# Kernel optimization log

Hardware: AMD Instinct MI355X
Metric: run time of the kernel (lower is better)

The kernel has to match this reference:

```python
import jax, jax.numpy as jnp
import numpy as np

NEG_BIG = -9e15
LEAKY_SLOPE = 0.01  # nn.LeakyReLU default

N, IN_DIM, HIDDEN_DIM, OUT_DIM = 16384, 512, 256, 128


def setup_inputs() -> dict:
    key = jax.random.key(0)
    ks = jax.random.split(key, 6)
    # He-ish init scaled like torch Linear defaults (uniform +-1/sqrt(fan_in))
    def lin_init(k, fan_in, fan_out):
        kw, kb = jax.random.split(k)
        bound = 1.0 / np.sqrt(fan_in)
        W = jax.random.uniform(kw, (fan_in, fan_out), jnp.float32, -bound, bound)
        b = jax.random.uniform(kb, (fan_out,), jnp.float32, -bound, bound)
        return W, b
    W1, b1 = lin_init(ks[0], IN_DIM, HIDDEN_DIM)
    W2, b2 = lin_init(ks[1], HIDDEN_DIM, OUT_DIM)
    x = jax.random.normal(ks[2], (N, IN_DIM), jnp.float32)
    return {
        "x": x,
        "g": 0,  # unused graph arg in the executed forward path
        "W1": W1, "b1": b1,
        "W2": W2, "b2": b2,
        "alpha": jnp.array([0.1], jnp.float32),
        "beta": jnp.array([0.9], jnp.float32),
    }


def _sim_agg(x):
    # adj: [N, N] dense similarity
    adj = jnp.matmul(x, x.T)
    a = jnp.where(adj > 0, adj, jnp.float32(NEG_BIG))
    sim1 = jax.nn.softmax(a, axis=1)
    return jnp.matmul(sim1, x)


def reference(x, g, W1, b1, W2, b2, alpha, beta):
    # dropout is inactive in eval mode (F.dropout with training=False)
    h = jnp.matmul(x, W1) + b1
    h = jnp.where(h >= 0, h, LEAKY_SLOPE * h)  # LeakyReLU
    h = jnp.matmul(h, W2) + b2                 # [N, out_dim]
    out = alpha * _sim_agg(h) + beta * h
    return jax.nn.log_softmax(out, axis=1)
```

## Files before the change

### kernel.cpp

```cpp
#include <hip/hip_runtime.h>
#include <hip/hip_bf16.h>

typedef __bf16 bf16_t;
typedef __bf16 bf16x8 __attribute__((ext_vector_type(8)));
typedef __bf16 bf16x4 __attribute__((ext_vector_type(4)));
typedef __bf16 bf16x2 __attribute__((ext_vector_type(2)));
typedef float f32x4 __attribute__((ext_vector_type(4)));
typedef float f32x2 __attribute__((ext_vector_type(2)));
typedef unsigned short u16;

#define NROWS 16384
#define KDIM  512
#define HID   256
#define ODIM  128
#define KS    8

__device__ __forceinline__ f32x4 mfma16(bf16x8 a, bf16x8 b, f32x4 c) {
  return __builtin_amdgcn_mfma_f32_16x16x32_bf16(a, b, c, 0, 0, 0);
}

__device__ __forceinline__ void dma16(const void* g, void* l) {
  __builtin_amdgcn_global_load_lds(
      (const __attribute__((address_space(1))) unsigned int*)g,
      (__attribute__((address_space(3))) unsigned int*)l, 16, 0, 0);
}

__global__ __launch_bounds__(256) void prep(const float* __restrict__ x,
                                            const float* __restrict__ W1,
                                            const float* __restrict__ W2,
                                            bf16_t* __restrict__ xb,
                                            bf16_t* __restrict__ W1T,
                                            bf16_t* __restrict__ W2T) {
  int t = blockIdx.x * 256 + threadIdx.x;
  int stride = gridDim.x * 256;
  for (int e = t; e < NROWS * KDIM / 4; e += stride) {
    f32x4 v = *(const f32x4*)(x + (size_t)e * 4);
    bf16x4 pk;
    pk[0] = (bf16_t)v[0]; pk[1] = (bf16_t)v[1];
    pk[2] = (bf16_t)v[2]; pk[3] = (bf16_t)v[3];
    *(bf16x4*)(xb + (size_t)e * 4) = pk;
  }
  for (int e = t; e < HID * KDIM; e += stride) {
    int n = e >> 9, k = e & 511;
    W1T[e] = (bf16_t)W1[k * HID + n];
  }
  for (int e = t; e < ODIM * HID; e += stride) {
    int n = e >> 8, k = e & 255;
    W2T[e] = (bf16_t)W2[k * ODIM + n];
  }
}

__global__ __launch_bounds__(256) void gemm1(const bf16_t* __restrict__ xb,
                                             const bf16_t* __restrict__ W1T,
                                             const float* __restrict__ b1,
                                             bf16_t* __restrict__ h1) {
  __shared__ u16 As[128 * 40];
  __shared__ u16 Bs[64 * 40];
  int tid = threadIdx.x;
  int lane = tid & 63, w = tid >> 6;
  int r = lane & 15, q = lane >> 4;
  int wm = w & 1, wn = w >> 1;
  int mbase = blockIdx.x * 128, nbase = blockIdx.y * 64;

  f32x4 acc[4][2];
#pragma unroll
  for (int ms = 0; ms < 4; ms++)
#pragma unroll
    for (int ns = 0; ns < 2; ns++) acc[ms][ns] = (f32x4){0.f, 0.f, 0.f, 0.f};

  for (int kb = 0; kb < KDIM; kb += 32) {
#pragma unroll
    for (int i = 0; i < 2; i++) {
      int g = tid + 256 * i;
      int rr = g >> 2, c = (g & 3) * 8;
      *(bf16x8*)&As[rr * 40 + c] =
          *(const bf16x8*)(xb + (size_t)(mbase + rr) * KDIM + kb + c);
    }
    {
      int rr = tid >> 2, c = (tid & 3) * 8;
      *(bf16x8*)&Bs[rr * 40 + c] =
          *(const bf16x8*)(W1T + (size_t)(nbase + rr) * KDIM + kb + c);
    }
    __syncthreads();
    bf16x8 af[4], bfr[2];
#pragma unroll
    for (int ms = 0; ms < 4; ms++)
      af[ms] = *(bf16x8*)&As[(wm * 64 + ms * 16 + r) * 40 + q * 8];
#pragma unroll
    for (int ns = 0; ns < 2; ns++)
      bfr[ns] = *(bf16x8*)&Bs[(wn * 32 + ns * 16 + r) * 40 + q * 8];
#pragma unroll
    for (int ms = 0; ms < 4; ms++)
#pragma unroll
      for (int ns = 0; ns < 2; ns++)
        acc[ms][ns] = mfma16(af[ms], bfr[ns], acc[ms][ns]);
    __syncthreads();
  }
#pragma unroll
  for (int ns = 0; ns < 2; ns++) {
    int col = nbase + wn * 32 + ns * 16 + r;
    float bias = b1[col];
#pragma unroll
    for (int ms = 0; ms < 4; ms++) {
      int row0 = mbase + wm * 64 + ms * 16 + q * 4;
#pragma unroll
      for (int reg = 0; reg < 4; reg++) {
        float v = acc[ms][ns][reg] + bias;
        v = v >= 0.f ? v : 0.01f * v;
        h1[(size_t)(row0 + reg) * HID + col] = (bf16_t)v;
      }
    }
  }
}

__global__ __launch_bounds__(256) void gemm2(const bf16_t* __restrict__ h1,
                                             const bf16_t* __restrict__ W2T,
                                             const float* __restrict__ b2,
                                             bf16_t* __restrict__ hb,
                                             bf16_t* __restrict__ hT) {
  __shared__ u16 As[128 * 40];
  __shared__ u16 Bs[64 * 40];
  int tid = threadIdx.x;
  int lane = tid & 63, w = tid >> 6;
  int r = lane & 15, q = lane >> 4;
  int wm = w & 1, wn = w >> 1;
  int mbase = blockIdx.x * 128, nbase = blockIdx.y * 64;

  f32x4 acc[4][2];
#pragma unroll
  for (int ms = 0; ms < 4; ms++)
#pragma unroll
    for (int ns = 0; ns < 2; ns++) acc[ms][ns] = (f32x4){0.f, 0.f, 0.f, 0.f};

  for (int kb = 0; kb < HID; kb += 32) {
#pragma unroll
    for (int i = 0; i < 2; i++) {
      int g = tid + 256 * i;
      int rr = g >> 2, c = (g & 3) * 8;
      *(bf16x8*)&As[rr * 40 + c] =
          *(const bf16x8*)(h1 + (size_t)(mbase + rr) * HID + kb + c);
    }
    {
      int rr = tid >> 2, c = (tid & 3) * 8;
      *(bf16x8*)&Bs[rr * 40 + c] =
          *(const bf16x8*)(W2T + (size_t)(nbase + rr) * HID + kb + c);
    }
    __syncthreads();
    bf16x8 af[4], bfr[2];
#pragma unroll
    for (int ms = 0; ms < 4; ms++)
      af[ms] = *(bf16x8*)&As[(wm * 64 + ms * 16 + r) * 40 + q * 8];
#pragma unroll
    for (int ns = 0; ns < 2; ns++)
      bfr[ns] = *(bf16x8*)&Bs[(wn * 32 + ns * 16 + r) * 40 + q * 8];
#pragma unroll
    for (int ms = 0; ms < 4; ms++)
#pragma unroll
      for (int ns = 0; ns < 2; ns++)
        acc[ms][ns] = mfma16(af[ms], bfr[ns], acc[ms][ns]);
    __syncthreads();
  }
#pragma unroll
  for (int ns = 0; ns < 2; ns++) {
    int col = nbase + wn * 32 + ns * 16 + r;
    float bias = b2[col];
#pragma unroll
    for (int ms = 0; ms < 4; ms++) {
      int row0 = mbase + wm * 64 + ms * 16 + q * 4;
      bf16x4 pk;
#pragma unroll
      for (int reg = 0; reg < 4; reg++) {
        float v = acc[ms][ns][reg] + bias;
        hb[(size_t)(row0 + reg) * ODIM + col] = (bf16_t)v;
        pk[reg] = (bf16_t)v;
      }
      *(bf16x4*)(hT + (size_t)col * NROWS + row0) = pk;
    }
  }
}

__global__ __launch_bounds__(256, 4) void flash(const bf16_t* __restrict__ hb,
                                                const bf16_t* __restrict__ hT,
                                                bf16_t* __restrict__ OpA,
                                                bf16_t* __restrict__ OpB,
                                                float* __restrict__ Ml) {
  __shared__ __align__(16) u16 KA[8 * 512];
  __shared__ __align__(16) u16 KT[2][8 * 512];
  __shared__ __align__(16) u16 Pm[4 * 32 * 40];

  int tid = threadIdx.x;
  int lane = tid & 63, w = tid >> 6;
  int r = lane & 15, q = lane >> 4;
  int ksplit = blockIdx.x >> 7;
  int qtile = blockIdx.x & 127;
  int qbase = qtile * 128 + w * 32;
  int kbase = ksplit * (NROWS / KS);
  const int niter = (NROWS / KS) / 32;

  const char* gbase;
  size_t jmul;
  int ginc;
  u16* dbase;
  if (w < 2) {
    gbase = (const char*)(hb + (size_t)(kbase + w * 16 + r) * ODIM + q * 8);
    jmul = 32 * 2;
    ginc = 32 * ODIM * 2;
    dbase = KA + w * 4 * 512;
  } else {
    gbase = (const char*)(hT + (size_t)((w - 2) * 64 + r) * NROWS + kbase + q * 8);
    jmul = (size_t)16 * NROWS * 2;
    ginc = 32 * 2;
    dbase = KT[0] + (w - 2) * 4 * 512;
  }

  bf16x8 qf[2][4];
#pragma unroll
  for (int qt = 0; qt < 2; qt++) {
    int qrow = qbase + qt * 16 + r;
#pragma unroll
    for (int kk = 0; kk < 4; kk++)
      qf[qt][kk] = *(const bf16x8*)(hb + (size_t)qrow * ODIM + kk * 32 + q * 8);
  }

  f32x4 oa[8][2];
#pragma unroll
  for (int m8 = 0; m8 < 8; m8++)
#pragma unroll
    for (int qt = 0; qt < 2; qt++) oa[m8][qt] = (f32x4){0.f, 0.f, 0.f, 0.f};
  float m_run[2] = {0.f, 0.f}, l_run[2] = {0.f, 0.f};

#pragma unroll
  for (int j = 0; j < 4; j++) dma16(gbase + j * jmul, dbase + j * 512);
  gbase += ginc;

  for (int it = 0; it < niter; it++) {
    __syncthreads();

    f32x4 s[2][2];
#pragma unroll
    for (int mt = 0; mt < 2; mt++)
#pragma unroll
      for (int qt = 0; qt < 2; qt++) s[mt][qt] = (f32x4){0.f, 0.f, 0.f, 0.f};
#pragma unroll
    for (int mt = 0; mt < 2; mt++)
#pragma unroll
      for (int kk = 0; kk < 4; kk++) {
        bf16x8 af = *(bf16x8*)&KA[(mt * 4 + kk) * 512 + lane * 8];
        s[mt][0] = mfma16(af, qf[0][kk], s[mt][0]);
        s[mt][1] = mfma16(af, qf[1][kk], s[mt][1]);
      }
    __syncthreads();

    if (it + 1 < niter) {
      u16* d = dbase;
      if (w >= 2) d += ((it + 1) & 1) * 4096;
#pragma unroll
      for (int j = 0; j < 4; j++) dma16(gbase + j * jmul, d + j * 512);
      gbase += ginc;
    }

    float mx[2];
#pragma unroll
    for (int qt = 0; qt < 2; qt++) {
      float m = m_run[qt];
#pragma unroll
      for (int mt = 0; mt < 2; mt++)
#pragma unroll
        for (int reg = 0; reg < 4; reg++) {
          float v = s[mt][qt][reg];
          m = v > 0.f ? fmaxf(m, v) : m;
        }
      m = fmaxf(m, __shfl_xor(m, 16, 64));
      m = fmaxf(m, __shfl_xor(m, 32, 64));
      mx[qt] = m;
    }
    if (__any(mx[0] > m_run[0] || mx[1] > m_run[1])) {
      float sc0 = __expf(m_run[0] - mx[0]);
      float sc1 = __expf(m_run[1] - mx[1]);
      m_run[0] = mx[0]; m_run[1] = mx[1];
      l_run[0] *= sc0; l_run[1] *= sc1;
#pragma unroll
      for (int m8 = 0; m8 < 8; m8++)
#pragma unroll
        for (int reg = 0; reg < 4; reg++) {
          oa[m8][0][reg] *= sc0;
          oa[m8][1][reg] *= sc1;
        }
    }
#pragma unroll
    for (int qt = 0; qt < 2; qt++) {
      float rs = 0.f;
      bf16x4 pk[2];
#pragma unroll
      for (int mt = 0; mt < 2; mt++)
#pragma unroll
        for (int reg = 0; reg < 4; reg++) {
          float v = s[mt][qt][reg];
          float p = v > 0.f ? __expf(v - m_run[qt]) : 0.f;
          rs += p;
          pk[mt][reg] = (bf16_t)p;
        }
      rs += __shfl_xor(rs, 16, 64);
      rs += __shfl_xor(rs, 32, 64);
      l_run[qt] += rs;
#pragma unroll
      for (int mt = 0; mt < 2; mt++)
        *(bf16x4*)&Pm[w * 1280 + (qt * 16 + r) * 40 + mt * 16 + q * 4] = pk[mt];
    }

    bf16x8 pf0 = *(bf16x8*)&Pm[w * 1280 + r * 40 + q * 8];
    bf16x8 pf1 = *(bf16x8*)&Pm[w * 1280 + (16 + r) * 40 + q * 8];
    const u16* kt = KT[it & 1];
#pragma unroll
    for (int m8 = 0; m8 < 8; m8++) {
      bf16x8 af = *(bf16x8*)&kt[m8 * 512 + lane * 8];
      oa[m8][0] = mfma16(af, pf0, oa[m8][0]);
      oa[m8][1] = mfma16(af, pf1, oa[m8][1]);
    }
  }

  bf16_t* op = ksplit < 6 ? OpA + (size_t)ksplit * NROWS * ODIM
                          : OpB + (size_t)(ksplit - 6) * NROWS * ODIM;
#pragma unroll
  for (int qt = 0; qt < 2; qt++) {
    int row = qbase + qt * 16 + r;
#pragma unroll
    for (int m8 = 0; m8 < 8; m8++) {
      bf16x4 pk;
#pragma unroll
      for (int reg = 0; reg < 4; reg++) pk[reg] = (bf16_t)oa[m8][qt][reg];
      *(bf16x4*)(op + (size_t)row * ODIM + m8 * 16 + q * 4) = pk;
    }
    if (q == 0) {
      Ml[(ksplit * NROWS + row) * 2 + 0] = m_run[qt];
      Ml[(ksplit * NROWS + row) * 2 + 1] = l_run[qt];
    }
  }
}

__global__ __launch_bounds__(256) void merge_ls(const bf16_t* __restrict__ OpA,
                                                const bf16_t* __restrict__ OpB,
                                                const float* __restrict__ Ml,
                                                const bf16_t* __restrict__ hbf,
                                                const float* __restrict__ alpha_p,
                                                const float* __restrict__ beta_p,
                                                float* __restrict__ out) {
  int tid = threadIdx.x, lane = tid & 63, w = tid >> 6;
  float al = alpha_p[0], be = beta_p[0];
  for (int i = 0; i < 8; i++) {
    int row = blockIdx.x * 32 + w * 8 + i;
    float mk[KS], lk[KS], ak[KS];
    float M = 0.f;
#pragma unroll
    for (int ksp = 0; ksp < KS; ksp++) {
      mk[ksp] = Ml[(ksp * NROWS + row) * 2 + 0];
      lk[ksp] = Ml[(ksp * NROWS + row) * 2 + 1];
      M = fmaxf(M, mk[ksp]);
    }
    float lt = 0.f;
#pragma unroll
    for (int ksp = 0; ksp < KS; ksp++) {
      ak[ksp] = __expf(mk[ksp] - M);
      lt += lk[ksp] * ak[ksp];
    }
    float inv = al / lt;
    int d0 = lane * 2;
    float a0 = 0.f, a1 = 0.f;
#pragma unroll
    for (int ksp = 0; ksp < KS; ksp++) {
      const bf16_t* op = ksp < 6 ? OpA + (size_t)ksp * NROWS * ODIM
                                 : OpB + (size_t)(ksp - 6) * NROWS * ODIM;
      bf16x2 v = *(const bf16x2*)(op + (size_t)row * ODIM + d0);
      a0 += ak[ksp] * (float)v[0];
      a1 += ak[ksp] * (float)v[1];
    }
    bf16x2 hv = *(const bf16x2*)(hbf + (size_t)row * ODIM + d0);
    float v0 = inv * a0 + be * (float)hv[0];
    float v1 = inv * a1 + be * (float)hv[1];
    float mxv = fmaxf(v0, v1);
#pragma unroll
    for (int off = 1; off < 64; off <<= 1) mxv = fmaxf(mxv, __shfl_xor(mxv, off, 64));
    float se = __expf(v0 - mxv) + __expf(v1 - mxv);
#pragma unroll
    for (int off = 1; off < 64; off <<= 1) se += __shfl_xor(se, off, 64);
    float lz = mxv + __logf(se);
    f32x2 st = {v0 - lz, v1 - lz};
    *(f32x2*)(out + (size_t)row * ODIM + d0) = st;
  }
}

extern "C" void kernel_launch(void* const* d_in, const int* in_sizes, int n_in,
                              void* d_out, int out_size, void* d_ws,
                              size_t ws_size, hipStream_t stream) {
  const float* x     = (const float*)d_in[0];
  const float* W1    = (const float*)d_in[2];
  const float* b1    = (const float*)d_in[3];
  const float* W2    = (const float*)d_in[4];
  const float* b2    = (const float*)d_in[5];
  const float* alpha = (const float*)d_in[6];
  const float* beta  = (const float*)d_in[7];

  char* ws = (char*)d_ws;
  bf16_t* xb  = (bf16_t*)(ws + 0);
  bf16_t* W1T = (bf16_t*)(ws + 16777216);
  bf16_t* W2T = (bf16_t*)(ws + 17039360);
  bf16_t* h1  = (bf16_t*)(ws + 17104896);
  bf16_t* hbf = (bf16_t*)(ws + 25493504);
  bf16_t* hT  = (bf16_t*)(ws + 29687808);
  float*  Ml  = (float*)(ws + 33882112);
  bf16_t* OpB = (bf16_t*)(ws + 34930688);
  bf16_t* OpA = (bf16_t*)(ws + 0);
  float* outp = (float*)d_out;

  prep<<<1024, 256, 0, stream>>>(x, W1, W2, xb, W1T, W2T);
  gemm1<<<dim3(128, 4), 256, 0, stream>>>(xb, W1T, b1, h1);
  gemm2<<<dim3(128, 2), 256, 0, stream>>>(h1, W2T, b2, hbf, hT);
  flash<<<128 * KS, 256, 0, stream>>>(hbf, hT, OpA, OpB, Ml);
  merge_ls<<<512, 256, 0, stream>>>(OpA, OpB, Ml, hbf, alpha, beta, outp);
}
```

Measured before the change: 364.3 us.

## Replace online softmax max with Cauchy-Schwarz row bound and double-buffer key tiles

A new rowstat kernel computes each row's squared norm and a global maximum squared norm. The flash kernel then uses the fixed per-row bound sqrt(|h_i|^2 * max|h_j|^2) in place of a running max. This removes the per-iteration max reduction, the cross-lane shuffles and the accumulator rescaling, and it also simplifies the merge step to plain sums. The key tile KA is now double-buffered, which drops one barrier per iteration, and the loop is unrolled by two. The P scratch tile uses an XOR swizzle instead of padding. The risk is exp underflow when the bound sits far above a row's true maximum, plus the cost of an extra small kernel launch and an atomic.

```diff
diff --git a/kernel.cpp b/kernel.cpp
--- a/kernel.cpp
+++ b/kernel.cpp
@@ -30,9 +30,11 @@
                                             const float* __restrict__ W2,
                                             bf16_t* __restrict__ xb,
                                             bf16_t* __restrict__ W1T,
-                                            bf16_t* __restrict__ W2T) {
+                                            bf16_t* __restrict__ W2T,
+                                            float* __restrict__ gmax) {
   int t = blockIdx.x * 256 + threadIdx.x;
   int stride = gridDim.x * 256;
+  if (t == 0) *gmax = 0.f;
   for (int e = t; e < NROWS * KDIM / 4; e += stride) {
     f32x4 v = *(const f32x4*)(x + (size_t)e * 4);
     bf16x4 pk;
@@ -179,14 +181,39 @@
   }
 }
 
+__global__ __launch_bounds__(256) void rowstat(const bf16_t* __restrict__ hb,
+                                               float* __restrict__ Mrow,
+                                               float* __restrict__ gmax) {
+  int row = blockIdx.x * 256 + threadIdx.x;
+  const bf16x8* p = (const bf16x8*)(hb + (size_t)row * ODIM);
+  float n2 = 0.f;
+#pragma unroll
+  for (int i = 0; i < 16; i++) {
+    bf16x8 v = p[i];
+#pragma unroll
+    for (int j = 0; j < 8; j++) {
+      float f = (float)v[j];
+      n2 += f * f;
+    }
+  }
+  Mrow[row] = n2;
+  float m = n2;
+#pragma unroll
+  for (int off = 1; off < 64; off <<= 1) m = fmaxf(m, __shfl_xor(m, off, 64));
+  if ((threadIdx.x & 63) == 0)
+    atomicMax((unsigned int*)gmax, __float_as_uint(m));
+}
+
 __global__ __launch_bounds__(256, 4) void flash(const bf16_t* __restrict__ hb,
                                                 const bf16_t* __restrict__ hT,
+                                                const float* __restrict__ Mrow,
+                                                const float* __restrict__ gmax,
                                                 bf16_t* __restrict__ OpA,
                                                 bf16_t* __restrict__ OpB,
                                                 float* __restrict__ Ml) {
-  __shared__ __align__(16) u16 KA[8 * 512];
-  __shared__ __align__(16) u16 KT[2][8 * 512];
-  __shared__ __align__(16) u16 Pm[4 * 32 * 40];
+  __shared__ __align__(16) u16 KA[2][4096];
+  __shared__ __align__(16) u16 KT[2][4096];
+  __shared__ __align__(16) u16 Pm[4096];
 
   int tid = threadIdx.x;
   int lane = tid & 63, w = tid >> 6;
@@ -195,28 +222,32 @@
   int qtile = blockIdx.x & 127;
   int qbase = qtile * 128 + w * 32;
   int kbase = ksplit * (NROWS / KS);
-  const int niter = (NROWS / KS) / 32;
 
   const char* gbase;
   size_t jmul;
-  int ginc;
-  u16* dbase;
+  long ginc;
+  u16 *d0, *d1;
   if (w < 2) {
     gbase = (const char*)(hb + (size_t)(kbase + w * 16 + r) * ODIM + q * 8);
-    jmul = 32 * 2;
+    jmul = 64;
     ginc = 32 * ODIM * 2;
-    dbase = KA + w * 4 * 512;
+    d0 = &KA[0][w * 2048];
+    d1 = &KA[1][w * 2048];
   } else {
     gbase = (const char*)(hT + (size_t)((w - 2) * 64 + r) * NROWS + kbase + q * 8);
     jmul = (size_t)16 * NROWS * 2;
-    ginc = 32 * 2;
-    dbase = KT[0] + (w - 2) * 4 * 512;
+    ginc = 64;
+    d0 = &KT[0][(w - 2) * 2048];
+    d1 = &KT[1][(w - 2) * 2048];
   }
 
   bf16x8 qf[2][4];
+  float mi[2];
+  float gm = gmax[0];
 #pragma unroll
   for (int qt = 0; qt < 2; qt++) {
     int qrow = qbase + qt * 16 + r;
+    mi[qt] = sqrtf(Mrow[qrow] * gm);
 #pragma unroll
     for (int kk = 0; kk < 4; kk++)
       qf[qt][kk] = *(const bf16x8*)(hb + (size_t)qrow * ODIM + kk * 32 + q * 8);
@@ -227,102 +258,73 @@
   for (int m8 = 0; m8 < 8; m8++)
 #pragma unroll
     for (int qt = 0; qt < 2; qt++) oa[m8][qt] = (f32x4){0.f, 0.f, 0.f, 0.f};
-  float m_run[2] = {0.f, 0.f}, l_run[2] = {0.f, 0.f};
-
-#pragma unroll
-  for (int j = 0; j < 4; j++) dma16(gbase + j * jmul, dbase + j * 512);
+  float lpart[2] = {0.f, 0.f};
+
+  u16* pw = &Pm[w * 1024];
+  int sw = (r & 3) * 8;
+
+#pragma unroll
+  for (int j = 0; j < 4; j++) dma16(gbase + j * jmul, d0 + j * 512);
   gbase += ginc;
 
-  for (int it = 0; it < niter; it++) {
-    __syncthreads();
-
-    f32x4 s[2][2];
-#pragma unroll
-    for (int mt = 0; mt < 2; mt++)
-#pragma unroll
-      for (int qt = 0; qt < 2; qt++) s[mt][qt] = (f32x4){0.f, 0.f, 0.f, 0.f};
-#pragma unroll
-    for (int mt = 0; mt < 2; mt++)
-#pragma unroll
-      for (int kk = 0; kk < 4; kk++) {
-        bf16x8 af = *(bf16x8*)&KA[(mt * 4 + kk) * 512 + lane * 8];
-        s[mt][0] = mfma16(af, qf[0][kk], s[mt][0]);
-        s[mt][1] = mfma16(af, qf[1][kk], s[mt][1]);
-      }
-    __syncthreads();
-
-    if (it + 1 < niter) {
-      u16* d = dbase;
-      if (w >= 2) d += ((it + 1) & 1) * 4096;
-#pragma unroll
-      for (int j = 0; j < 4; j++) dma16(gbase + j * jmul, d + j * 512);
-      gbase += ginc;
-    }
-
-    float mx[2];
-#pragma unroll
-    for (int qt = 0; qt < 2; qt++) {
-      float m = m_run[qt];
-#pragma unroll
-      for (int mt = 0; mt < 2; mt++)
-#pragma unroll
-        for (int reg = 0; reg < 4; reg++) {
-          float v = s[mt][qt][reg];
-          m = v > 0.f ? fmaxf(m, v) : m;
-        }
-      m = fmaxf(m, __shfl_xor(m, 16, 64));
-      m = fmaxf(m, __shfl_xor(m, 32, 64));
-      mx[qt] = m;
-    }
-    if (__any(mx[0] > m_run[0] || mx[1] > m_run[1])) {
-      float sc0 = __expf(m_run[0] - mx[0]);
-      float sc1 = __expf(m_run[1] - mx[1]);
-      m_run[0] = mx[0]; m_run[1] = mx[1];
-      l_run[0] *= sc0; l_run[1] *= sc1;
-#pragma unroll
-      for (int m8 = 0; m8 < 8; m8++)
-#pragma unroll
-        for (int reg = 0; reg < 4; reg++) {
-          oa[m8][0][reg] *= sc0;
-          oa[m8][1][reg] *= sc1;
-        }
-    }
-#pragma unroll
-    for (int qt = 0; qt < 2; qt++) {
-      float rs = 0.f;
-      bf16x4 pk[2];
-#pragma unroll
-      for (int mt = 0; mt < 2; mt++)
-#pragma unroll
-        for (int reg = 0; reg < 4; reg++) {
-          float v = s[mt][qt][reg];
-          float p = v > 0.f ? __expf(v - m_run[qt]) : 0.f;
-          rs += p;
-          pk[mt][reg] = (bf16_t)p;
-        }
-      rs += __shfl_xor(rs, 16, 64);
-      rs += __shfl_xor(rs, 32, 64);
-      l_run[qt] += rs;
-#pragma unroll
-      for (int mt = 0; mt < 2; mt++)
-        *(bf16x4*)&Pm[w * 1280 + (qt * 16 + r) * 40 + mt * 16 + q * 4] = pk[mt];
-    }
-
-    bf16x8 pf0 = *(bf16x8*)&Pm[w * 1280 + r * 40 + q * 8];
-    bf16x8 pf1 = *(bf16x8*)&Pm[w * 1280 + (16 + r) * 40 + q * 8];
-    const u16* kt = KT[it & 1];
-#pragma unroll
-    for (int m8 = 0; m8 < 8; m8++) {
-      bf16x8 af = *(bf16x8*)&kt[m8 * 512 + lane * 8];
-      oa[m8][0] = mfma16(af, pf0, oa[m8][0]);
-      oa[m8][1] = mfma16(af, pf1, oa[m8][1]);
-    }
-  }
+#define FLASH_ITER(BUF, PF)                                                   \
+  {                                                                           \
+    __syncthreads();              \
+    if (PF) {                                                                 \
+      u16* dd = (BUF) ? d0 : d1;                                              \
+      _Pragma("unroll") for (int j = 0; j < 4; j++)                           \
+          dma16(gbase + j * jmul, dd + j * 512);                              \
+      gbase += ginc;                                                          \
+    }                                                                         \
+    f32x4 s[2][2];                                                            \
+    _Pragma("unroll") for (int mt = 0; mt < 2; mt++)                          \
+        _Pragma("unroll") for (int qt = 0; qt < 2; qt++)                      \
+            s[mt][qt] = (f32x4){0.f, 0.f, 0.f, 0.f};                          \
+    _Pragma("unroll") for (int mt = 0; mt < 2; mt++)                          \
+        _Pragma("unroll") for (int kk = 0; kk < 4; kk++) {                    \
+      bf16x8 af = *(bf16x8*)&KA[BUF][(mt * 4 + kk) * 512 + lane * 8];         \
+      s[mt][0] = mfma16(af, qf[0][kk], s[mt][0]);                             \
+      s[mt][1] = mfma16(af, qf[1][kk], s[mt][1]);                             \
+    }                                                                         \
+    _Pragma("unroll") for (int qt = 0; qt < 2; qt++) {                        \
+      bf16x4 pk[2];                                                           \
+      float rsum = 0.f;                                                       \
+      _Pragma("unroll") for (int mt = 0; mt < 2; mt++)                        \
+          _Pragma("unroll") for (int reg = 0; reg < 4; reg++) {               \
+        float v = s[mt][qt][reg];                                             \
+        float p = v > 0.f ? __expf(v - mi[qt]) : 0.f;                         \
+        rsum += p;                                                            \
+        pk[mt][reg] = (bf16_t)p;                                              \
+      }                                                                       \
+      lpart[qt] += rsum;                                                      \
+      _Pragma("unroll") for (int mt = 0; mt < 2; mt++)                        \
+        *(bf16x4*)&pw[(qt * 16 + r) * 32 +                                    \
+                      (((mt * 16 + (q >> 1) * 8) ^ sw) + (q & 1) * 4)] =      \
+            pk[mt];                                                           \
+    }                                                                         \
+    bf16x8 pf0 = *(bf16x8*)&pw[r * 32 + ((q * 8) ^ sw)];                      \
+    bf16x8 pf1 = *(bf16x8*)&pw[(16 + r) * 32 + ((q * 8) ^ sw)];               \
+    _Pragma("unroll") for (int m8 = 0; m8 < 8; m8++) {                        \
+      bf16x8 af = *(bf16x8*)&KT[BUF][m8 * 512 + lane * 8];                    \
+      oa[m8][0] = mfma16(af, pf0, oa[m8][0]);                                 \
+      oa[m8][1] = mfma16(af, pf1, oa[m8][1]);                                 \
+    }                                                                         \
+  }
+
+#pragma unroll 1
+  for (int it2 = 0; it2 < 32; it2++) {
+    FLASH_ITER(0, true)
+    FLASH_ITER(1, (it2 < 31))
+  }
+#undef FLASH_ITER
 
   bf16_t* op = ksplit < 6 ? OpA + (size_t)ksplit * NROWS * ODIM
                           : OpB + (size_t)(ksplit - 6) * NROWS * ODIM;
 #pragma unroll
   for (int qt = 0; qt < 2; qt++) {
+    float l = lpart[qt];
+    l += __shfl_xor(l, 16, 64);
+    l += __shfl_xor(l, 32, 64);
     int row = qbase + qt * 16 + r;
 #pragma unroll
     for (int m8 = 0; m8 < 8; m8++) {
@@ -331,10 +333,7 @@
       for (int reg = 0; reg < 4; reg++) pk[reg] = (bf16_t)oa[m8][qt][reg];
       *(bf16x4*)(op + (size_t)row * ODIM + m8 * 16 + q * 4) = pk;
     }
-    if (q == 0) {
-      Ml[(ksplit * NROWS + row) * 2 + 0] = m_run[qt];
-      Ml[(ksplit * NROWS + row) * 2 + 1] = l_run[qt];
-    }
+    if (q == 0) Ml[ksplit * NROWS + row] = l;
   }
 }
 
@@ -349,20 +348,9 @@
   float al = alpha_p[0], be = beta_p[0];
   for (int i = 0; i < 8; i++) {
     int row = blockIdx.x * 32 + w * 8 + i;
-    float mk[KS], lk[KS], ak[KS];
-    float M = 0.f;
-#pragma unroll
-    for (int ksp = 0; ksp < KS; ksp++) {
-      mk[ksp] = Ml[(ksp * NROWS + row) * 2 + 0];
-      lk[ksp] = Ml[(ksp * NROWS + row) * 2 + 1];
-      M = fmaxf(M, mk[ksp]);
-    }
     float lt = 0.f;
 #pragma unroll
-    for (int ksp = 0; ksp < KS; ksp++) {
-      ak[ksp] = __expf(mk[ksp] - M);
-      lt += lk[ksp] * ak[ksp];
-    }
+    for (int ksp = 0; ksp < KS; ksp++) lt += Ml[ksp * NROWS + row];
     float inv = al / lt;
     int d0 = lane * 2;
     float a0 = 0.f, a1 = 0.f;
@@ -371,8 +359,8 @@
       const bf16_t* op = ksp < 6 ? OpA + (size_t)ksp * NROWS * ODIM
                                  : OpB + (size_t)(ksp - 6) * NROWS * ODIM;
       bf16x2 v = *(const bf16x2*)(op + (size_t)row * ODIM + d0);
-      a0 += ak[ksp] * (float)v[0];
-      a1 += ak[ksp] * (float)v[1];
+      a0 += (float)v[0];
+      a1 += (float)v[1];
     }
     bf16x2 hv = *(const bf16x2*)(hbf + (size_t)row * ODIM + d0);
     float v0 = inv * a0 + be * (float)hv[0];
@@ -401,20 +389,23 @@
   const float* beta  = (const float*)d_in[7];
 
   char* ws = (char*)d_ws;
-  bf16_t* xb  = (bf16_t*)(ws + 0);
-  bf16_t* W1T = (bf16_t*)(ws + 16777216);
-  bf16_t* W2T = (bf16_t*)(ws + 17039360);
-  bf16_t* h1  = (bf16_t*)(ws + 17104896);
-  bf16_t* hbf = (bf16_t*)(ws + 25493504);
-  bf16_t* hT  = (bf16_t*)(ws + 29687808);
-  float*  Ml  = (float*)(ws + 33882112);
-  bf16_t* OpB = (bf16_t*)(ws + 34930688);
-  bf16_t* OpA = (bf16_t*)(ws + 0);
-  float* outp = (float*)d_out;
-
-  prep<<<1024, 256, 0, stream>>>(x, W1, W2, xb, W1T, W2T);
+  bf16_t* xb   = (bf16_t*)(ws + 0);
+  bf16_t* W1T  = (bf16_t*)(ws + 16777216);
+  bf16_t* W2T  = (bf16_t*)(ws + 17039360);
+  bf16_t* h1   = (bf16_t*)(ws + 17104896);
+  bf16_t* hbf  = (bf16_t*)(ws + 25493504);
+  bf16_t* hT   = (bf16_t*)(ws + 29687808);
+  float*  Ml   = (float*)(ws + 33882112);
+  float*  Mrow = (float*)(ws + 34406400);
+  float*  gmax = (float*)(ws + 34471936);
+  bf16_t* OpB  = (bf16_t*)(ws + 34930688);
+  bf16_t* OpA  = (bf16_t*)(ws + 0);
+  float* outp  = (float*)d_out;
+
+  prep<<<1024, 256, 0, stream>>>(x, W1, W2, xb, W1T, W2T, gmax);
   gemm1<<<dim3(128, 4), 256, 0, stream>>>(xb, W1T, b1, h1);
   gemm2<<<dim3(128, 2), 256, 0, stream>>>(h1, W2T, b2, hbf, hT);
-  flash<<<128 * KS, 256, 0, stream>>>(hbf, hT, OpA, OpB, Ml);
+  rowstat<<<64, 256, 0, stream>>>(hbf, Mrow, gmax);
+  flash<<<128 * KS, 256, 0, stream>>>(hbf, hT, Mrow, gmax, OpA, OpB, Ml);
   merge_ls<<<512, 256, 0, stream>>>(OpA, OpB, Ml, hbf, alpha, beta, outp);
 }
```

After: 583.8 us. +60.3%, slower.
